# Kernel optimization log

Measured on AMD Instinct MI355X. Metric: run time of the kernel, lower is better.

Reference implementation:

```python
import jax, jax.numpy as jnp
import numpy as np

B, T, C, H = 16, 512, 1080, 20  # batch, seq, embd, heads; head_dim = C // H = 54

def setup_inputs() -> dict:
    key = jax.random.key(0)
    k1, k2, k3, k4, k5 = jax.random.split(key, 5)
    s = 0.02
    return {
        "x": jax.random.normal(k1, (B, T, C), dtype=jnp.float32),
        "W_attn": jax.random.normal(k2, (C, 3 * C), dtype=jnp.float32) * s,
        "b_attn": jax.random.normal(k3, (3 * C,), dtype=jnp.float32) * s,
        "W_proj": jax.random.normal(k4, (C, C), dtype=jnp.float32) * s,
        "b_proj": jax.random.normal(k5, (C,), dtype=jnp.float32) * s,
    }

def reference(x, W_attn, b_attn, W_proj, b_proj):
    Bb, Tt, Cc = x.shape
    hd = Cc // H
    qkv = jnp.einsum('btc,cd->btd', x, W_attn) + b_attn  # [B,T,3C]
    q, k, v = jnp.split(qkv, 3, axis=2)
    # [B,T,C] -> [B,H,T,hd]
    q = q.reshape(Bb, Tt, H, hd).transpose(0, 2, 1, 3)
    k = k.reshape(Bb, Tt, H, hd).transpose(0, 2, 1, 3)
    v = v.reshape(Bb, Tt, H, hd).transpose(0, 2, 1, 3)
    att = jnp.einsum('bhqd,bhkd->bhqk', q, k) * (1.0 / jnp.sqrt(jnp.float32(hd)))
    causal = jnp.tril(jnp.ones((Tt, Tt), dtype=bool))
    att = jnp.where(causal, att, -jnp.inf)
    att = jax.nn.softmax(att, axis=-1)
    y = jnp.einsum('bhqk,bhkd->bhqd', att, v)  # [B,H,T,hd]
    y = y.transpose(0, 2, 1, 3).reshape(Bb, Tt, Cc)
    return jnp.einsum('btc,cd->btd', y, W_proj) + b_proj
```

## Files before the change

### kernel.cpp

```cpp
#include <hip/hip_runtime.h>
#include <hip/hip_bf16.h>

#define B_   16
#define T_   512
#define C_   1080
#define H_   20
#define HD_  54
#define DP_  64
#define M_   (B_ * T_)
#define KP_  1088
#define NT_  17
#define NQKV_ 3840
#define NPRJ_ 1152
#define NBT_ (B_ * H_ * T_)

typedef short bf16x8 __attribute__((ext_vector_type(8)));
typedef float f32x4  __attribute__((ext_vector_type(4)));
typedef unsigned short u16x8 __attribute__((ext_vector_type(8)));

__device__ __forceinline__ void gload_lds16(const void* g, void* l) {
    __builtin_amdgcn_global_load_lds(
        (const __attribute__((address_space(1))) void*)g,
        (__attribute__((address_space(3))) void*)l,
        16, 0, 0);
}

__global__ __launch_bounds__(256) void cvt_pad(
    const float* __restrict__ src, __hip_bfloat16* __restrict__ dst)
{
    int idx = blockIdx.x * 256 + threadIdx.x;
    if (idx >= M_ * (KP_ / 4)) return;
    int m = idx / (KP_ / 4), c = idx - m * (KP_ / 4);
    ushort4 o;
    if (c < C_ / 4) {
        float4 v = *reinterpret_cast<const float4*>(src + (size_t)m * C_ + c * 4);
        o.x = __builtin_bit_cast(unsigned short, __float2bfloat16(v.x));
        o.y = __builtin_bit_cast(unsigned short, __float2bfloat16(v.y));
        o.z = __builtin_bit_cast(unsigned short, __float2bfloat16(v.z));
        o.w = __builtin_bit_cast(unsigned short, __float2bfloat16(v.w));
    } else {
        o.x = o.y = o.z = o.w = 0;
    }
    *reinterpret_cast<ushort4*>(reinterpret_cast<unsigned short*>(dst) + (size_t)m * KP_ + c * 4) = o;
}

__global__ __launch_bounds__(256) void transpose_wqkv(
    const float* __restrict__ W, __hip_bfloat16* __restrict__ Wt)
{
    __shared__ float tile[32][33];
    int n0 = blockIdx.x * 32, k0 = blockIdx.y * 32;
    int tx = threadIdx.x, ty = threadIdx.y;
    int np = n0 + tx;
    int which = np / 1280;
    int rem = np - which * 1280;
    int h = rem >> 6, d = rem & 63;
    int sn = which * C_ + h * HD_ + d;
    bool valid = d < HD_;
    #pragma unroll
    for (int i = 0; i < 32; i += 8) {
        int k = k0 + ty + i;
        tile[ty + i][tx] = (valid && k < C_) ? W[(size_t)k * (3 * C_) + sn] : 0.f;
    }
    __syncthreads();
    #pragma unroll
    for (int i = 0; i < 32; i += 8) {
        int n = n0 + ty + i, k = k0 + tx;
        Wt[(size_t)n * KP_ + k] = __float2bfloat16(tile[tx][ty + i]);
    }
}

__global__ __launch_bounds__(256) void transpose_w(
    const float* __restrict__ W, __hip_bfloat16* __restrict__ Wt,
    int K, int N, int Kp)
{
    __shared__ float tile[32][33];
    int n0 = blockIdx.x * 32, k0 = blockIdx.y * 32;
    int tx = threadIdx.x, ty = threadIdx.y;
    #pragma unroll
    for (int i = 0; i < 32; i += 8) {
        int k = k0 + ty + i, n = n0 + tx;
        tile[ty + i][tx] = (k < K && n < N) ? W[(size_t)k * N + n] : 0.f;
    }
    __syncthreads();
    #pragma unroll
    for (int i = 0; i < 32; i += 8) {
        int n = n0 + ty + i, k = k0 + tx;
        Wt[(size_t)n * Kp + k] = __float2bfloat16(tile[tx][ty + i]);
    }
}

__global__ __launch_bounds__(256) void build_bias(
    const float* __restrict__ b_attn, float* __restrict__ bp)
{
    int i = blockIdx.x * 256 + threadIdx.x;
    if (i < NQKV_) {
        int which = i / 1280, rem = i - which * 1280;
        int h = rem >> 6, d = rem & 63;
        float v = (d < HD_) ? b_attn[which * C_ + h * HD_ + d] : 0.f;
        if (which == 2 && d == 63) v = 1.0f;
        bp[i] = v;
    }
}

template<int MODE>
__global__ __launch_bounds__(256) void gemm_mfma(
    const unsigned short* __restrict__ A,
    const unsigned short* __restrict__ Bt,
    const float* __restrict__ bias,
    float* __restrict__ outP,
    unsigned short* __restrict__ outQ,
    unsigned short* __restrict__ outK,
    unsigned short* __restrict__ outV)
{
    __shared__ __align__(16) char smem[65536];

    const int tid  = threadIdx.x;
    const int lane = tid & 63;
    const int wv   = tid >> 6;
    const int wm   = (wv >> 1) * 64;
    const int wn   = (wv & 1) * 64;
    const int lr   = lane & 15;
    const int lk   = lane >> 4;

    const int gx  = gridDim.x;
    const int gy  = gridDim.y;
    const int id  = blockIdx.y * gx + blockIdx.x;
    const int xcd = id & 7;
    const int j   = id >> 3;
    const int mpc = gy >> 3;
    const int m0  = (xcd * mpc + j % mpc) * 128;
    const int n0  = (j / mpc) * 128;

    unsigned aOff[4], bOff[4];
    int ciB[4];
    #pragma unroll
    for (int it = 0; it < 4; ++it) {
        int ci = it * 256 + tid;
        int r = ci >> 3, p = ci & 7;
        int kc = p ^ (r & 7);
        aOff[it] = (unsigned)(m0 + r) * KP_ + kc * 8;
        bOff[it] = (unsigned)(n0 + r) * KP_ + kc * 8;
        ciB[it] = ci * 16;
    }
    int aRd[2][4], bRd[2][4];
    #pragma unroll
    for (int kk = 0; kk < 2; ++kk) {
        #pragma unroll
        for (int mi = 0; mi < 4; ++mi) {
            int row = wm + mi * 16 + lr;
            aRd[kk][mi] = row * 128 + ((kk * 4 + lk) ^ (row & 7)) * 16;
            int rowb = wn + mi * 16 + lr;
            bRd[kk][mi] = 16384 + rowb * 128 + ((kk * 4 + lk) ^ (rowb & 7)) * 16;
        }
    }

    f32x4 acc[4][4] = {};

    auto stage = [&](int buf, int kt) {
        const unsigned k0 = kt * 64;
        char* sb = smem + buf * 32768;
        #pragma unroll
        for (int it = 0; it < 4; ++it)
            gload_lds16(A + aOff[it] + k0, sb + ciB[it]);
        #pragma unroll
        for (int it = 0; it < 4; ++it)
            gload_lds16(Bt + bOff[it] + k0, sb + 16384 + ciB[it]);
    };

    stage(0, 0);
    for (int kt = 0; kt < NT_; ++kt) {
        const int c = kt & 1;
        if (kt + 1 < NT_) {
            stage(1 - c, kt + 1);
            asm volatile("s_waitcnt vmcnt(8)" ::: "memory");
        } else {
            asm volatile("s_waitcnt vmcnt(0)" ::: "memory");
        }
        __builtin_amdgcn_s_barrier();
        asm volatile("" ::: "memory");

        const char* base = smem + c * 32768;
        #pragma unroll
        for (int kk = 0; kk < 2; ++kk) {
            bf16x8 af[4], bfr[4];
            #pragma unroll
            for (int mi = 0; mi < 4; ++mi)
                af[mi] = *reinterpret_cast<const bf16x8*>(base + aRd[kk][mi]);
            #pragma unroll
            for (int ni = 0; ni < 4; ++ni)
                bfr[ni] = *reinterpret_cast<const bf16x8*>(base + bRd[kk][ni]);
            #pragma unroll
            for (int mi = 0; mi < 4; ++mi)
                #pragma unroll
                for (int ni = 0; ni < 4; ++ni)
                    acc[mi][ni] = __builtin_amdgcn_mfma_f32_16x16x32_bf16(
                        af[mi], bfr[ni], acc[mi][ni], 0, 0, 0);
        }
        asm volatile("" ::: "memory");
        __builtin_amdgcn_s_barrier();
    }

    if constexpr (MODE == 0) {
        #pragma unroll
        for (int mi = 0; mi < 4; ++mi) {
            int mrow = m0 + wm + mi * 16 + lk * 4;
            #pragma unroll
            for (int ni = 0; ni < 4; ++ni) {
                int n = n0 + wn + ni * 16 + lr;
                if (n < C_) {
                    float bs = bias[n];
                    #pragma unroll
                    for (int j2 = 0; j2 < 4; ++j2)
                        outP[(size_t)(mrow + j2) * C_ + n] = acc[mi][ni][j2] + bs;
                }
            }
        }
    } else {
        const int which = n0 / 1280;
        if (which < 2) {
            unsigned short* dst = which ? outK : outQ;
            #pragma unroll
            for (int mi = 0; mi < 4; ++mi) {
                int mg = m0 + wm + mi * 16 + lk * 4;
                int b = mg >> 9, t0 = mg & (T_ - 1);
                #pragma unroll
                for (int ni = 0; ni < 4; ++ni) {
                    int nl = wn + ni * 16 + lr;
                    int ng = n0 + nl - which * 1280;
                    int h = ng >> 6, d = ng & 63;
                    float bs = bias[n0 + nl];
                    size_t basei = ((size_t)(b * H_ + h) * T_ + t0) * DP_ + d;
                    #pragma unroll
                    for (int j2 = 0; j2 < 4; ++j2)
                        dst[basei + (size_t)j2 * DP_] = __builtin_bit_cast(unsigned short,
                            __float2bfloat16(acc[mi][ni][j2] + bs));
                }
            }
        } else {
            unsigned short* lt = (unsigned short*)smem;
            #pragma unroll
            for (int mi = 0; mi < 4; ++mi) {
                int ml = wm + mi * 16 + lk * 4;
                int mc = ml >> 3, mo = ml & 7;
                #pragma unroll
                for (int ni = 0; ni < 4; ++ni) {
                    int nl = wn + ni * 16 + lr;
                    float bs = bias[n0 + nl];
                    ushort4 pk;
                    pk.x = __builtin_bit_cast(unsigned short, __float2bfloat16(acc[mi][ni][0] + bs));
                    pk.y = __builtin_bit_cast(unsigned short, __float2bfloat16(acc[mi][ni][1] + bs));
                    pk.z = __builtin_bit_cast(unsigned short, __float2bfloat16(acc[mi][ni][2] + bs));
                    pk.w = __builtin_bit_cast(unsigned short, __float2bfloat16(acc[mi][ni][3] + bs));
                    int slot = mc ^ ((nl >> 3) & 15);
                    *reinterpret_cast<ushort4*>(lt + nl * 136 + slot * 8 + mo) = pk;
                }
            }
            __syncthreads();
            #pragma unroll
            for (int it = 0; it < 8; ++it) {
                int idx = it * 256 + tid;
                int c2 = idx >> 4, j2 = idx & 15;
                int slot = j2 ^ ((c2 >> 3) & 15);
                u16x8 v = *reinterpret_cast<const u16x8*>(lt + c2 * 136 + slot * 8);
                int ng = n0 + c2 - 2560;
                int h = ng >> 6, d = ng & 63;
                int mg = m0 + j2 * 8;
                int b = mg >> 9, t = mg & (T_ - 1);
                *reinterpret_cast<u16x8*>(outV + ((size_t)(b * H_ + h) * DP_ + d) * T_ + t) = v;
            }
        }
    }
}

__global__ __launch_bounds__(256) void attn_mfma(
    const unsigned short* __restrict__ Q, const unsigned short* __restrict__ K,
    const unsigned short* __restrict__ Vt, __hip_bfloat16* __restrict__ Y)
{
    __shared__ __align__(16) char kvs[16384];
    __shared__ __align__(16) unsigned short ps[4][16][72];

    const int tid  = threadIdx.x;
    const int lane = tid & 63;
    const int wv   = tid >> 6;
    const int lq   = lane & 15;
    const int lg   = lane >> 4;
    const int bh   = blockIdx.y;
    const int qt   = blockIdx.x;
    const int qbase = qt * 64;
    const float cs = 0.13608276348795434f * 1.44269504f;

    bf16x8 qf[2];
    {
        const unsigned short* qp = Q + ((size_t)bh * T_ + qbase + wv * 16 + lq) * DP_;
        qf[0] = *reinterpret_cast<const bf16x8*>(qp + lg * 8);
        qf[1] = *reinterpret_cast<const bf16x8*>(qp + 32 + lg * 8);
    }

    unsigned kOff[2], vOff[2];
    int ciB[2];
    #pragma unroll
    for (int it = 0; it < 2; ++it) {
        int ci = it * 256 + tid;
        int r = ci >> 3, p = ci & 7;
        int pc = p ^ (r & 7);
        kOff[it] = (unsigned)(r * DP_ + pc * 8);
        vOff[it] = (unsigned)(r * T_ + pc * 8);
        ciB[it] = ci * 16;
    }
    const unsigned short* Kb = K  + (size_t)bh * T_ * DP_;
    const unsigned short* Vb = Vt + (size_t)bh * DP_ * T_;

    f32x4 o[4] = {};
    unsigned short* pbase = &ps[wv][0][0];
    const int nt = qt + 1;

    for (int kt = 0; kt < nt; ++kt) {
        const int kbase = kt * 64;
        #pragma unroll
        for (int it = 0; it < 2; ++it)
            gload_lds16(Kb + kOff[it] + (unsigned)kbase * DP_, kvs + ciB[it]);
        #pragma unroll
        for (int it = 0; it < 2; ++it)
            gload_lds16(Vb + vOff[it] + (unsigned)kbase, kvs + 8192 + ciB[it]);
        __syncthreads();

        f32x4 s[4] = {};
        #pragma unroll
        for (int dc = 0; dc < 2; ++dc) {
            #pragma unroll
            for (int ni = 0; ni < 4; ++ni) {
                int row = ni * 16 + lq;
                int ch  = (dc * 4 + lg) ^ (row & 7);
                bf16x8 kf = *reinterpret_cast<const bf16x8*>(kvs + row * 128 + ch * 16);
                s[ni] = __builtin_amdgcn_mfma_f32_16x16x32_bf16(qf[dc], kf, s[ni], 0, 0, 0);
            }
        }

        if (kt == qt) {
            #pragma unroll
            for (int ni = 0; ni < 4; ++ni) {
                int kg = kbase + ni * 16 + lq;
                #pragma unroll
                for (int j = 0; j < 4; ++j) {
                    int qg = qbase + wv * 16 + lg * 4 + j;
                    s[ni][j] = (kg > qg) ? -3.0e38f : s[ni][j];
                }
            }
        }
        #pragma unroll
        for (int ni = 0; ni < 4; ++ni) {
            #pragma unroll
            for (int j = 0; j < 4; ++j) {
                float p = exp2f(s[ni][j] * cs);
                int qr = lg * 4 + j;
                int cidx = (ni * 2 + (lq >> 3)) ^ (qr & 7);
                pbase[qr * 72 + cidx * 8 + (lq & 7)] =
                    __builtin_bit_cast(unsigned short, __float2bfloat16(p));
            }
        }

        asm volatile("s_waitcnt lgkmcnt(0)" ::: "memory");
        __builtin_amdgcn_sched_barrier(0);

        #pragma unroll
        for (int dc = 0; dc < 2; ++dc) {
            int cc = (dc * 4 + lg) ^ (lq & 7);
            bf16x8 pf = *reinterpret_cast<const bf16x8*>(pbase + lq * 72 + cc * 8);
            #pragma unroll
            for (int ni = 0; ni < 4; ++ni) {
                int row = ni * 16 + lq;
                int ch  = (dc * 4 + lg) ^ (row & 7);
                bf16x8 vf = *reinterpret_cast<const bf16x8*>(kvs + 8192 + row * 128 + ch * 16);
                o[ni] = __builtin_amdgcn_mfma_f32_16x16x32_bf16(pf, vf, o[ni], 0, 0, 0);
            }
        }
        __syncthreads();
    }

    const int b = bh / H_, h = bh - b * H_;
    #pragma unroll
    for (int j = 0; j < 4; ++j) {
        float l = __shfl(o[3][j], (lane & 48) | 15, 64);
        float inv = 1.f / l;
        int t = qbase + wv * 16 + lg * 4 + j;
        #pragma unroll
        for (int ni = 0; ni < 4; ++ni) {
            int d = ni * 16 + lq;
            if (d < HD_)
                Y[((size_t)b * T_ + t) * KP_ + h * HD_ + d] =
                    __float2bfloat16(o[ni][j] * inv);
        }
    }
}

extern "C" void kernel_launch(void* const* d_in, const int* in_sizes, int n_in,
                              void* d_out, int out_size, void* d_ws, size_t ws_size,
                              hipStream_t stream)
{
    const float* x      = (const float*)d_in[0];
    const float* W_attn = (const float*)d_in[1];
    const float* b_attn = (const float*)d_in[2];
    const float* W_proj = (const float*)d_in[3];
    const float* b_proj = (const float*)d_in[4];
    float* out = (float*)d_out;

    __hip_bfloat16* xb = (__hip_bfloat16*)d_ws;
    unsigned short* qb = (unsigned short*)(xb + (size_t)M_ * KP_);
    unsigned short* kb = qb + (size_t)NBT_ * DP_;
    unsigned short* vtb = kb + (size_t)NBT_ * DP_;
    __hip_bfloat16* wta = (__hip_bfloat16*)(vtb + (size_t)NBT_ * DP_);
    __hip_bfloat16* wtp = wta + (size_t)NQKV_ * KP_;
    float* bp = (float*)(wtp + (size_t)NPRJ_ * KP_);
    __hip_bfloat16* yb = xb;

    cvt_pad<<<(M_ * (KP_ / 4) + 255) / 256, 256, 0, stream>>>(x, xb);
    transpose_wqkv<<<dim3(NQKV_ / 32, KP_ / 32), dim3(32, 8), 0, stream>>>(W_attn, wta);
    transpose_w<<<dim3(NPRJ_ / 32, KP_ / 32), dim3(32, 8), 0, stream>>>(
        W_proj, wtp, C_, C_, KP_);
    build_bias<<<(NQKV_ + 255) / 256, 256, 0, stream>>>(b_attn, bp);

    gemm_mfma<1><<<dim3(NQKV_ / 128, M_ / 128), 256, 0, stream>>>(
        (const unsigned short*)xb, (const unsigned short*)wta, bp,
        nullptr, qb, kb, vtb);

    attn_mfma<<<dim3(T_ / 64, B_ * H_), 256, 0, stream>>>(qb, kb, vtb, yb);

    gemm_mfma<0><<<dim3(NPRJ_ / 128, M_ / 128), 256, 0, stream>>>(
        (const unsigned short*)yb, (const unsigned short*)wtp, b_proj,
        out, nullptr, nullptr, nullptr);
}
```

Before: 196.6 us.

## Use 256x256 tile, 8-wave QKV GEMM with interleaved prefetch pipeline

Replaces the 128x128 QKV projection GEMM with a dedicated 256x256-tile kernel using 512 threads, 128KB LDS double buffering, staged global-to-LDS prefetch interleaved with MFMA phases, and s_setprio around MFMA bursts. Larger tiles raise arithmetic intensity and cut redundant A/B loads. The V-transpose epilogue is split into two halves to fit LDS. Risks lower occupancy and a grid of 15x32 blocks that may balance poorly across CUs.

```diff
diff --git a/kernel.cpp b/kernel.cpp
--- a/kernel.cpp
+++ b/kernel.cpp
@@ -25,6 +25,10 @@
         16, 0, 0);
 }
 
+__device__ __forceinline__ unsigned short f2b(float x) {
+    return __builtin_bit_cast(unsigned short, __float2bfloat16(x));
+}
+
 __global__ __launch_bounds__(256) void cvt_pad(
     const float* __restrict__ src, __hip_bfloat16* __restrict__ dst)
 {
@@ -34,10 +38,7 @@
     ushort4 o;
     if (c < C_ / 4) {
         float4 v = *reinterpret_cast<const float4*>(src + (size_t)m * C_ + c * 4);
-        o.x = __builtin_bit_cast(unsigned short, __float2bfloat16(v.x));
-        o.y = __builtin_bit_cast(unsigned short, __float2bfloat16(v.y));
-        o.z = __builtin_bit_cast(unsigned short, __float2bfloat16(v.z));
-        o.w = __builtin_bit_cast(unsigned short, __float2bfloat16(v.w));
+        o.x = f2b(v.x); o.y = f2b(v.y); o.z = f2b(v.z); o.w = f2b(v.w);
     } else {
         o.x = o.y = o.z = o.w = 0;
     }
@@ -102,15 +103,173 @@
     }
 }
 
-template<int MODE>
-__global__ __launch_bounds__(256) void gemm_mfma(
+__global__ __launch_bounds__(512, 2) void gemm256(
     const unsigned short* __restrict__ A,
     const unsigned short* __restrict__ Bt,
     const float* __restrict__ bias,
-    float* __restrict__ outP,
     unsigned short* __restrict__ outQ,
     unsigned short* __restrict__ outK,
     unsigned short* __restrict__ outV)
+{
+    __shared__ __align__(16) char smem[131072];
+
+    const int tid  = threadIdx.x;
+    const int lane = tid & 63;
+    const int wv   = tid >> 6;
+    const int wr   = wv >> 2;
+    const int wc   = wv & 3;
+    const int lq   = lane & 15;
+    const int lg   = lane >> 4;
+
+    const int id  = blockIdx.y * 15 + blockIdx.x;
+    const int xcd = id & 7;
+    const int j   = id >> 3;
+    const int m0  = (xcd * 4 + (j & 3)) * 256;
+    const int n0  = (j >> 2) * 256;
+
+    unsigned gA[2], gB[2];
+    const int ld0 = tid * 16, ld1 = tid * 16 + 8192;
+    #pragma unroll
+    for (int i = 0; i < 2; ++i) {
+        int ci = tid + i * 512;
+        int r  = ci >> 3;
+        int kc = (ci & 7) ^ (r & 7);
+        gA[i] = (unsigned)(m0 + r) * KP_ + kc * 8;
+        gB[i] = (unsigned)(n0 + r) * KP_ + kc * 8;
+    }
+    const unsigned HALFSTEP = 128u * KP_;
+
+    auto stage = [&](int buf, int hIdx, unsigned k0) {
+        char* sb = smem + buf * 65536 +
+                   (hIdx < 2 ? hIdx * 16384 : 32768 + (hIdx - 2) * 16384);
+        const unsigned short* sp = (hIdx < 2) ? A : Bt;
+        unsigned extra = (hIdx & 1) ? HALFSTEP : 0u;
+        gload_lds16(sp + ((hIdx < 2) ? gA[0] : gB[0]) + extra + k0, sb + ld0);
+        gload_lds16(sp + ((hIdx < 2) ? gA[1] : gB[1]) + extra + k0, sb + ld1);
+    };
+
+    const int s0 = (lg ^ (lq & 7)) * 16;
+    const int s1 = ((4 + lg) ^ (lq & 7)) * 16;
+    const int aBase = wr * 16384 + lq * 128;
+    const int bBase = 32768 + (wc >> 1) * 16384 + (wc & 1) * 8192 + lq * 128;
+
+    f32x4 acc[8][4] = {};
+
+    stage(0, 0, 0); stage(0, 1, 0); stage(0, 2, 0); stage(0, 3, 0);
+    asm volatile("s_waitcnt vmcnt(0)" ::: "memory");
+    __builtin_amdgcn_s_barrier();
+
+    for (int t = 0; t < NT_; ++t) {
+        const int cur = t & 1, nxt = cur ^ 1;
+        const bool pf = (t + 1 < NT_);
+        const unsigned k0n = (unsigned)(t + 1) * 64;
+        const char* Ab = smem + cur * 65536 + aBase;
+        const char* Bb = smem + cur * 65536 + bBase;
+
+        bf16x8 bfr[4][2];
+        #pragma unroll
+        for (int p = 0; p < 4; ++p) {
+            if (p == 0 && pf) { stage(nxt, 0, k0n); stage(nxt, 1, k0n); }
+            if (p == 1 && pf) { stage(nxt, 2, k0n); stage(nxt, 3, k0n); }
+
+            bf16x8 af[2][2];
+            #pragma unroll
+            for (int i = 0; i < 2; ++i) {
+                int mi = p * 2 + i;
+                af[0][i] = *reinterpret_cast<const bf16x8*>(Ab + mi * 2048 + s0);
+                af[1][i] = *reinterpret_cast<const bf16x8*>(Ab + mi * 2048 + s1);
+            }
+            if (p == 0) {
+                #pragma unroll
+                for (int ni = 0; ni < 4; ++ni) {
+                    bfr[ni][0] = *reinterpret_cast<const bf16x8*>(Bb + ni * 2048 + s0);
+                    bfr[ni][1] = *reinterpret_cast<const bf16x8*>(Bb + ni * 2048 + s1);
+                }
+            }
+
+            __builtin_amdgcn_s_barrier();
+            asm volatile("s_waitcnt lgkmcnt(0)" ::: "memory");
+            __builtin_amdgcn_sched_barrier(0);
+            __builtin_amdgcn_s_setprio(1);
+            #pragma unroll
+            for (int kk = 0; kk < 2; ++kk)
+                #pragma unroll
+                for (int i = 0; i < 2; ++i)
+                    #pragma unroll
+                    for (int ni = 0; ni < 4; ++ni)
+                        acc[p * 2 + i][ni] = __builtin_amdgcn_mfma_f32_16x16x32_bf16(
+                            af[kk][i], bfr[ni][kk], acc[p * 2 + i][ni], 0, 0, 0);
+            __builtin_amdgcn_s_setprio(0);
+            if (p == 3) asm volatile("s_waitcnt vmcnt(0)" ::: "memory");
+            __builtin_amdgcn_s_barrier();
+        }
+    }
+
+    const int which = n0 / 1280;
+    if (which < 2) {
+        unsigned short* dst = which ? outK : outQ;
+        #pragma unroll
+        for (int mi = 0; mi < 8; ++mi) {
+            int mg = m0 + wr * 128 + mi * 16 + lg * 4;
+            int b = mg >> 9, t0 = mg & (T_ - 1);
+            #pragma unroll
+            for (int ni = 0; ni < 4; ++ni) {
+                int nl = wc * 64 + ni * 16 + lq;
+                int ng = n0 + nl - which * 1280;
+                int h = ng >> 6, d = ng & 63;
+                float bs = bias[n0 + nl];
+                size_t basei = ((size_t)(b * H_ + h) * T_ + t0) * DP_ + d;
+                #pragma unroll
+                for (int j2 = 0; j2 < 4; ++j2)
+                    dst[basei + (size_t)j2 * DP_] = f2b(acc[mi][ni][j2] + bs);
+            }
+        }
+    } else {
+        unsigned short* lt = (unsigned short*)smem;
+        #pragma unroll
+        for (int hm = 0; hm < 2; ++hm) {
+            if (hm == 1) __syncthreads();
+            if (wr == hm) {
+                #pragma unroll
+                for (int mi = 0; mi < 8; ++mi) {
+                    int ml = mi * 16 + lg * 4;
+                    int mc = ml >> 3, mo = ml & 7;
+                    #pragma unroll
+                    for (int ni = 0; ni < 4; ++ni) {
+                        int nl = wc * 64 + ni * 16 + lq;
+                        float bs = bias[n0 + nl];
+                        ushort4 pk;
+                        pk.x = f2b(acc[mi][ni][0] + bs);
+                        pk.y = f2b(acc[mi][ni][1] + bs);
+                        pk.z = f2b(acc[mi][ni][2] + bs);
+                        pk.w = f2b(acc[mi][ni][3] + bs);
+                        int slot = mc ^ ((nl >> 3) & 15);
+                        *reinterpret_cast<ushort4*>(lt + nl * 136 + slot * 8 + mo) = pk;
+                    }
+                }
+            }
+            __syncthreads();
+            #pragma unroll
+            for (int it = 0; it < 8; ++it) {
+                int idx = it * 512 + tid;
+                int c2 = idx >> 4, j2 = idx & 15;
+                int slot = j2 ^ ((c2 >> 3) & 15);
+                u16x8 v = *reinterpret_cast<const u16x8*>(lt + c2 * 136 + slot * 8);
+                int ng = n0 + c2 - 2560;
+                int h = ng >> 6, d = ng & 63;
+                int mg = m0 + hm * 128 + j2 * 8;
+                int b = mg >> 9, t = mg & (T_ - 1);
+                *reinterpret_cast<u16x8*>(outV + ((size_t)(b * H_ + h) * DP_ + d) * T_ + t) = v;
+            }
+        }
+    }
+}
+
+__global__ __launch_bounds__(256) void gemm_mfma_p(
+    const unsigned short* __restrict__ A,
+    const unsigned short* __restrict__ Bt,
+    const float* __restrict__ bias,
+    float* __restrict__ outP)
 {
     __shared__ __align__(16) char smem[65536];
 
@@ -200,73 +359,17 @@
         __builtin_amdgcn_s_barrier();
     }
 
-    if constexpr (MODE == 0) {
-        #pragma unroll
-        for (int mi = 0; mi < 4; ++mi) {
-            int mrow = m0 + wm + mi * 16 + lk * 4;
-            #pragma unroll
-            for (int ni = 0; ni < 4; ++ni) {
-                int n = n0 + wn + ni * 16 + lr;
-                if (n < C_) {
-                    float bs = bias[n];
-                    #pragma unroll
-                    for (int j2 = 0; j2 < 4; ++j2)
-                        outP[(size_t)(mrow + j2) * C_ + n] = acc[mi][ni][j2] + bs;
-                }
-            }
-        }
-    } else {
-        const int which = n0 / 1280;
-        if (which < 2) {
-            unsigned short* dst = which ? outK : outQ;
-            #pragma unroll
-            for (int mi = 0; mi < 4; ++mi) {
-                int mg = m0 + wm + mi * 16 + lk * 4;
-                int b = mg >> 9, t0 = mg & (T_ - 1);
-                #pragma unroll
-                for (int ni = 0; ni < 4; ++ni) {
-                    int nl = wn + ni * 16 + lr;
-                    int ng = n0 + nl - which * 1280;
-                    int h = ng >> 6, d = ng & 63;
-                    float bs = bias[n0 + nl];
-                    size_t basei = ((size_t)(b * H_ + h) * T_ + t0) * DP_ + d;
-                    #pragma unroll
-                    for (int j2 = 0; j2 < 4; ++j2)
-                        dst[basei + (size_t)j2 * DP_] = __builtin_bit_cast(unsigned short,
-                            __float2bfloat16(acc[mi][ni][j2] + bs));
-                }
-            }
-        } else {
-            unsigned short* lt = (unsigned short*)smem;
-            #pragma unroll
-            for (int mi = 0; mi < 4; ++mi) {
-                int ml = wm + mi * 16 + lk * 4;
-                int mc = ml >> 3, mo = ml & 7;
-                #pragma unroll
-                for (int ni = 0; ni < 4; ++ni) {
-                    int nl = wn + ni * 16 + lr;
-                    float bs = bias[n0 + nl];
-                    ushort4 pk;
-                    pk.x = __builtin_bit_cast(unsigned short, __float2bfloat16(acc[mi][ni][0] + bs));
-                    pk.y = __builtin_bit_cast(unsigned short, __float2bfloat16(acc[mi][ni][1] + bs));
-                    pk.z = __builtin_bit_cast(unsigned short, __float2bfloat16(acc[mi][ni][2] + bs));
-                    pk.w = __builtin_bit_cast(unsigned short, __float2bfloat16(acc[mi][ni][3] + bs));
-                    int slot = mc ^ ((nl >> 3) & 15);
-                    *reinterpret_cast<ushort4*>(lt + nl * 136 + slot * 8 + mo) = pk;
-                }
-            }
-            __syncthreads();
-            #pragma unroll
-            for (int it = 0; it < 8; ++it) {
-                int idx = it * 256 + tid;
-                int c2 = idx >> 4, j2 = idx & 15;
-                int slot = j2 ^ ((c2 >> 3) & 15);
-                u16x8 v = *reinterpret_cast<const u16x8*>(lt + c2 * 136 + slot * 8);
-                int ng = n0 + c2 - 2560;
-                int h = ng >> 6, d = ng & 63;
-                int mg = m0 + j2 * 8;
-                int b = mg >> 9, t = mg & (T_ - 1);
-                *reinterpret_cast<u16x8*>(outV + ((size_t)(b * H_ + h) * DP_ + d) * T_ + t) = v;
+    #pragma unroll
+    for (int mi = 0; mi < 4; ++mi) {
+        int mrow = m0 + wm + mi * 16 + lk * 4;
+        #pragma unroll
+        for (int ni = 0; ni < 4; ++ni) {
+            int n = n0 + wn + ni * 16 + lr;
+            if (n < C_) {
+                float bs = bias[n];
+                #pragma unroll
+                for (int j2 = 0; j2 < 4; ++j2)
+                    outP[(size_t)(mrow + j2) * C_ + n] = acc[mi][ni][j2] + bs;
             }
         }
     }
@@ -354,8 +457,7 @@
                 float p = exp2f(s[ni][j] * cs);
                 int qr = lg * 4 + j;
                 int cidx = (ni * 2 + (lq >> 3)) ^ (qr & 7);
-                pbase[qr * 72 + cidx * 8 + (lq & 7)] =
-                    __builtin_bit_cast(unsigned short, __float2bfloat16(p));
+                pbase[qr * 72 + cidx * 8 + (lq & 7)] = f2b(p);
             }
         }
 
@@ -419,13 +521,12 @@
         W_proj, wtp, C_, C_, KP_);
     build_bias<<<(NQKV_ + 255) / 256, 256, 0, stream>>>(b_attn, bp);
 
-    gemm_mfma<1><<<dim3(NQKV_ / 128, M_ / 128), 256, 0, stream>>>(
+    gemm256<<<dim3(NQKV_ / 256, M_ / 256), 512, 0, stream>>>(
         (const unsigned short*)xb, (const unsigned short*)wta, bp,
-        nullptr, qb, kb, vtb);
+        qb, kb, vtb);
 
     attn_mfma<<<dim3(T_ / 64, B_ * H_), 256, 0, stream>>>(qb, kb, vtb, yb);
 
-    gemm_mfma<0><<<dim3(NPRJ_ / 128, M_ / 128), 256, 0, stream>>>(
-        (const unsigned short*)yb, (const unsigned short*)wtp, b_proj,
-        out, nullptr, nullptr, nullptr);
-}
+    gemm_mfma_p<<<dim3(NPRJ_ / 128, M_ / 128), 256, 0, stream>>>(
+        (const unsigned short*)yb, (const unsigned short*)wtp, b_proj, out);
+}
```

Measured after the change: 185.2 us. 1.06x faster.
